# Optimization experiments

Hardware: AMD Instinct MI355X
Metric: run time of the kernel (lower is better)

The kernel has to match this reference:

```python
import jax, jax.numpy as jnp
import numpy as np

EPS = 1e-7  # K.epsilon()

def setup_inputs() -> dict:
    key = jax.random.key(0)
    k1, k2, k3 = jax.random.split(key, 3)
    B, T, D = 32, 2048, 512
    x = jax.random.normal(k1, (B, T, D), dtype=jnp.float32)
    W = jax.random.normal(k2, (D, D), dtype=jnp.float32) * (1.0 / np.sqrt(D))
    b = jnp.zeros((D,), dtype=jnp.float32)
    u = jax.random.normal(k3, (D,), dtype=jnp.float32) * (1.0 / np.sqrt(D))
    return {"x": x, "W": W, "b": b, "u": u}

def reference(x, W, b, u):
    # uit = tanh(x @ W + b)  -> [B, T, D]
    uit = jnp.tanh(jnp.einsum('btd,de->bte', x, W) + b)
    # scores: sum over feature dim of uit * u -> [B, T]
    ait = jnp.einsum('btd,d->bt', uit, u)
    # exp + normalize over T (no mask); matches original exp/sum form
    a = jnp.exp(ait)
    a = a / (jnp.sum(a, axis=1, keepdims=True) + EPS)
    # weighted sum pooling over T -> [B, D]
    return jnp.einsum('btd,bt->bd', x, a)
```

## Files before the change

### kernel.cpp

```cpp
#include <hip/hip_runtime.h>
#include <math.h>

#define D_DIM 512

typedef short short8v __attribute__((ext_vector_type(8)));
typedef unsigned short ushort8v __attribute__((ext_vector_type(8)));
typedef float f32x16 __attribute__((ext_vector_type(16)));

__device__ inline unsigned short f2bf(float f) {
    union { float f; unsigned int u; } a; a.f = f;
    unsigned int u = a.u;
    unsigned int r = (u + 0x7fffu + ((u >> 16) & 1u)) >> 16;
    return (unsigned short)r;
}

__device__ inline float fast_tanh(float y) {
    float e2 = __expf(2.f * y);
    return 1.f - __fdividef(2.f, e2 + 1.f);
}

#define ASYNC_CP16(gp, lp) \
    __builtin_amdgcn_global_load_lds( \
        (const __attribute__((address_space(1))) void*)(gp), \
        (__attribute__((address_space(3))) void*)(lp), 16, 0, 0)

__global__ __launch_bounds__(256) void wt_kernel(const float* __restrict__ W,
                                                 unsigned short* __restrict__ Wb2) {
    __shared__ __align__(16) unsigned short lbuf[16384];
    const int s = blockIdx.x;
    const int tid = threadIdx.x;
    #pragma unroll
    for (int i = 0; i < 16; ++i) {
        int flat = tid + i * 256;
        int kr = flat >> 7;
        int e4 = (flat & 127) * 4;
        float4 v = *(const float4*)(W + (size_t)(s * 32 + kr) * D_DIM + e4);
        int ks = kr >> 4, half = (kr >> 3) & 1, j = kr & 7;
        float vv[4] = {v.x, v.y, v.z, v.w};
        #pragma unroll
        for (int q = 0; q < 4; ++q) {
            int e = e4 + q, nt = e >> 5, nl = e & 31;
            lbuf[(((nt * 2 + ks) * 2 + half) * 32 + nl) * 8 + j] = f2bf(vv[q]);
        }
    }
    __syncthreads();
    #pragma unroll
    for (int i = 0; i < 8; ++i) {
        int c = tid + i * 256;
        *(ushort8v*)(Wb2 + (size_t)s * 16384 + c * 8) = *(const ushort8v*)&lbuf[c * 8];
    }
}

constexpr int XLDE = 40;

__global__ __launch_bounds__(256, 2) void gemm_ait_mfma(
    const float* __restrict__ x, const unsigned short* __restrict__ Wb2,
    const float* __restrict__ bias, const float* __restrict__ u,
    float* __restrict__ ait)
{
    __shared__ __align__(16) unsigned short wsh[2][16384];
    __shared__ __align__(16) unsigned short xs[2][64 * XLDE];
    __shared__ float rowpart[4][64];

    const int tid  = threadIdx.x;
    const int wave = tid >> 6;
    const int lane = tid & 63;
    const int half = lane >> 5;
    const int nl   = lane & 31;
    const int m0   = blockIdx.x * 64;

    f32x16 acc[2][4];
    #pragma unroll
    for (int mi = 0; mi < 2; ++mi)
        #pragma unroll
        for (int ni = 0; ni < 4; ++ni)
            #pragma unroll
            for (int r = 0; r < 16; ++r) acc[mi][ni][r] = 0.f;

    const int xr = tid >> 2;
    const int xc = tid & 3;
    const float* xbase = x + (size_t)(m0 + xr) * D_DIM + xc * 8;

    #pragma unroll
    for (int i = 0; i < 8; ++i)
        ASYNC_CP16(Wb2 + tid * 8 + i * 2048, &wsh[0][tid * 8 + i * 2048]);
    float4 px0 = *(const float4*)(xbase);
    float4 px1 = *(const float4*)(xbase + 4);

    for (int s = 0; s < 16; ++s) {
        const int pb = s & 1;
        {
            ushort8v pk;
            pk[0] = f2bf(px0.x); pk[1] = f2bf(px0.y); pk[2] = f2bf(px0.z); pk[3] = f2bf(px0.w);
            pk[4] = f2bf(px1.x); pk[5] = f2bf(px1.y); pk[6] = f2bf(px1.z); pk[7] = f2bf(px1.w);
            *(ushort8v*)&xs[pb][xr * XLDE + xc * 8] = pk;
        }
        __syncthreads();

        if (s + 1 < 16) {
            const unsigned short* wsrc = Wb2 + (size_t)(s + 1) * 16384;
            #pragma unroll
            for (int i = 0; i < 8; ++i)
                ASYNC_CP16(wsrc + tid * 8 + i * 2048, &wsh[1 - pb][tid * 8 + i * 2048]);
            px0 = *(const float4*)(xbase + (s + 1) * 32);
            px1 = *(const float4*)(xbase + (s + 1) * 32 + 4);
        }

        #pragma unroll
        for (int ks = 0; ks < 2; ++ks) {
            short8v af[2], bfr[4];
            #pragma unroll
            for (int mi = 0; mi < 2; ++mi)
                af[mi] = *(const short8v*)&xs[pb][(mi * 32 + nl) * XLDE + ks * 16 + half * 8];
            #pragma unroll
            for (int ni = 0; ni < 4; ++ni)
                bfr[ni] = *(const short8v*)&wsh[pb][(((wave * 4 + ni) * 2 + ks) * 2 + half) * 256 + nl * 8];
            #pragma unroll
            for (int mi = 0; mi < 2; ++mi)
                #pragma unroll
                for (int ni = 0; ni < 4; ++ni)
                    acc[mi][ni] = __builtin_amdgcn_mfma_f32_32x32x16_bf16(
                        af[mi], bfr[ni], acc[mi][ni], 0, 0, 0);
        }
    }

    float rowsum[2][16];
    #pragma unroll
    for (int mi = 0; mi < 2; ++mi)
        #pragma unroll
        for (int r = 0; r < 16; ++r) rowsum[mi][r] = 0.f;

    #pragma unroll
    for (int mi = 0; mi < 2; ++mi) {
        #pragma unroll
        for (int ni = 0; ni < 4; ++ni) {
            int col = wave * 128 + ni * 32 + nl;
            float be = bias[col], ue = u[col];
            #pragma unroll
            for (int r = 0; r < 16; ++r)
                rowsum[mi][r] += fast_tanh(acc[mi][ni][r] + be) * ue;
        }
    }
    #pragma unroll
    for (int mi = 0; mi < 2; ++mi)
        #pragma unroll
        for (int r = 0; r < 16; ++r) {
            float v = rowsum[mi][r];
            v += __shfl_xor(v, 1, 64);
            v += __shfl_xor(v, 2, 64);
            v += __shfl_xor(v, 4, 64);
            v += __shfl_xor(v, 8, 64);
            v += __shfl_xor(v, 16, 64);
            rowsum[mi][r] = v;
        }
    if (nl == 0) {
        #pragma unroll
        for (int mi = 0; mi < 2; ++mi)
            #pragma unroll
            for (int r = 0; r < 16; ++r) {
                int row = mi * 32 + (r & 3) + 8 * (r >> 2) + 4 * half;
                rowpart[wave][row] = rowsum[mi][r];
            }
    }
    __syncthreads();
    if (tid < 64)
        ait[m0 + tid] = rowpart[0][tid] + rowpart[1][tid] + rowpart[2][tid] + rowpart[3][tid];
}

__global__ __launch_bounds__(256) void gemm_ait_f32(
    const float* __restrict__ x, const float* __restrict__ W,
    const float* __restrict__ bias, const float* __restrict__ u,
    float* __restrict__ ait)
{
    __shared__ float xsf[64][68];
    __shared__ float wshf[64][132];
    const int tid = threadIdx.x;
    const int tx = tid & 15, ty = tid >> 4;
    const int m0 = blockIdx.x * 64;
    float rowsum[4] = {0.f, 0.f, 0.f, 0.f};
    for (int e0 = 0; e0 < D_DIM; e0 += 128) {
        float acc[4][8];
        #pragma unroll
        for (int i = 0; i < 4; ++i)
            #pragma unroll
            for (int j = 0; j < 8; ++j) acc[i][j] = 0.f;
        for (int kc = 0; kc < D_DIM; kc += 64) {
            #pragma unroll
            for (int i = 0; i < 4; ++i) {
                int idx = tid + i * 256;
                int r = idx >> 4, c = (idx & 15) * 4;
                *(float4*)&xsf[r][c] = *(const float4*)(x + (size_t)(m0 + r) * D_DIM + kc + c);
            }
            #pragma unroll
            for (int i = 0; i < 8; ++i) {
                int idx = tid + i * 256;
                int r = idx >> 5, c = (idx & 31) * 4;
                *(float4*)&wshf[r][c] = *(const float4*)(W + (size_t)(kc + r) * D_DIM + e0 + c);
            }
            __syncthreads();
            #pragma unroll 4
            for (int k = 0; k < 64; ++k) {
                float xv[4];
                #pragma unroll
                for (int i = 0; i < 4; ++i) xv[i] = xsf[ty * 4 + i][k];
                float4 w0 = *(const float4*)&wshf[k][tx * 8];
                float4 w1 = *(const float4*)&wshf[k][tx * 8 + 4];
                #pragma unroll
                for (int i = 0; i < 4; ++i) {
                    acc[i][0] += xv[i] * w0.x; acc[i][1] += xv[i] * w0.y;
                    acc[i][2] += xv[i] * w0.z; acc[i][3] += xv[i] * w0.w;
                    acc[i][4] += xv[i] * w1.x; acc[i][5] += xv[i] * w1.y;
                    acc[i][6] += xv[i] * w1.z; acc[i][7] += xv[i] * w1.w;
                }
            }
            __syncthreads();
        }
        #pragma unroll
        for (int j = 0; j < 8; ++j) {
            int e = e0 + tx * 8 + j;
            float be = bias[e], ue = u[e];
            #pragma unroll
            for (int i = 0; i < 4; ++i) rowsum[i] += tanhf(acc[i][j] + be) * ue;
        }
    }
    float* red = &xsf[0][0];
    #pragma unroll
    for (int i = 0; i < 4; ++i) red[(ty * 4 + i) * 16 + tx] = rowsum[i];
    __syncthreads();
    if (tid < 64) {
        float s = 0.f;
        #pragma unroll
        for (int j = 0; j < 16; ++j) s += red[tid * 16 + j];
        ait[m0 + tid] = s;
    }
}

__global__ __launch_bounds__(256) void softmax_kernel(float* __restrict__ ait, int T)
{
    const int b = blockIdx.x;
    float* p = ait + (size_t)b * T;
    const int tid = threadIdx.x;
    float ev[8];
    float local = 0.f;
    #pragma unroll
    for (int i = 0; i < 8; ++i) {
        ev[i] = expf(p[tid + i * 256]);
        local += ev[i];
    }
    #pragma unroll
    for (int off = 32; off > 0; off >>= 1)
        local += __shfl_down(local, off, 64);
    __shared__ float wsum[4];
    const int wv = tid >> 6, lane = tid & 63;
    if (lane == 0) wsum[wv] = local;
    __syncthreads();
    float total = wsum[0] + wsum[1] + wsum[2] + wsum[3];
    float inv = 1.0f / (total + 1e-7f);
    #pragma unroll
    for (int i = 0; i < 8; ++i) p[tid + i * 256] = ev[i] * inv;
}

__device__ inline float4 pool_accum(const float* __restrict__ x,
                                    const float* __restrict__ a,
                                    int b, int c, int tid, int T) {
    const int th = tid >> 7;
    const int d = (tid & 127) * 4;
    const float* xp = x + ((size_t)b * T + c * 64) * D_DIM + d;
    const float* ap = a + (size_t)b * T + c * 64;
    float4 acc = {0.f, 0.f, 0.f, 0.f};
    #pragma unroll 8
    for (int t = th; t < 64; t += 2) {
        float s = ap[t];
        float4 xv = *(const float4*)(xp + (size_t)t * D_DIM);
        acc.x += xv.x * s; acc.y += xv.y * s;
        acc.z += xv.z * s; acc.w += xv.w * s;
    }
    return acc;
}

__global__ __launch_bounds__(256) void pool_partial_kernel(
    const float* __restrict__ x, const float* __restrict__ a,
    float* __restrict__ partial, int T)
{
    const int chunks = T >> 6;
    const int b = blockIdx.x / chunks;
    const int c = blockIdx.x % chunks;
    const int tid = threadIdx.x;
    float4 acc = pool_accum(x, a, b, c, tid, T);
    __shared__ float4 tmp[128];
    if ((tid >> 7) == 1) tmp[tid & 127] = acc;
    __syncthreads();
    if ((tid >> 7) == 0) {
        float4 o = tmp[tid];
        acc.x += o.x; acc.y += o.y; acc.z += o.z; acc.w += o.w;
        *(float4*)(partial + (size_t)blockIdx.x * D_DIM + tid * 4) = acc;
    }
}

__global__ __launch_bounds__(256) void pool_reduce_kernel(
    const float* __restrict__ partial, float* __restrict__ out, int chunks)
{
    const int b = blockIdx.x;
    const int tid = threadIdx.x;
    const int d = tid * 2;
    float2 acc = {0.f, 0.f};
    for (int c = 0; c < chunks; ++c) {
        float2 v = *(const float2*)(partial + ((size_t)b * chunks + c) * D_DIM + d);
        acc.x += v.x; acc.y += v.y;
    }
    *(float2*)(out + (size_t)b * D_DIM + d) = acc;
}

__global__ __launch_bounds__(256) void pool_atomic_kernel(
    const float* __restrict__ x, const float* __restrict__ a,
    float* __restrict__ out, int T)
{
    const int chunks = T >> 6;
    const int b = blockIdx.x / chunks;
    const int c = blockIdx.x % chunks;
    const int tid = threadIdx.x;
    float4 acc = pool_accum(x, a, b, c, tid, T);
    __shared__ float4 tmp[128];
    if ((tid >> 7) == 1) tmp[tid & 127] = acc;
    __syncthreads();
    if ((tid >> 7) == 0) {
        float4 o = tmp[tid];
        float* op = out + (size_t)b * D_DIM + tid * 4;
        atomicAdd(op + 0, acc.x + o.x);
        atomicAdd(op + 1, acc.y + o.y);
        atomicAdd(op + 2, acc.z + o.z);
        atomicAdd(op + 3, acc.w + o.w);
    }
}

extern "C" void kernel_launch(void* const* d_in, const int* in_sizes, int n_in,
                              void* d_out, int out_size, void* d_ws, size_t ws_size,
                              hipStream_t stream)
{
    const float* x    = (const float*)d_in[0];
    const float* W    = (const float*)d_in[1];
    const float* bias = (const float*)d_in[2];
    const float* u    = (const float*)d_in[3];
    float* out = (float*)d_out;

    const int Dd = in_sizes[2];
    const int M  = in_sizes[0] / Dd;
    const int B  = out_size / Dd;
    const int T  = M / B;
    const int chunks = T >> 6;

    const size_t wb_bytes   = (size_t)Dd * Dd * sizeof(unsigned short);
    const size_t ait_bytes  = (size_t)M * sizeof(float);
    const size_t part_bytes = (size_t)B * chunks * Dd * sizeof(float);

    if (ws_size >= wb_bytes + ait_bytes) {
        unsigned short* Wb2 = (unsigned short*)d_ws;
        float* ait = (float*)((char*)d_ws + wb_bytes);
        wt_kernel<<<dim3(16), dim3(256), 0, stream>>>(W, Wb2);
        gemm_ait_mfma<<<dim3(M / 64), dim3(256), 0, stream>>>(x, Wb2, bias, u, ait);
        softmax_kernel<<<dim3(B), dim3(256), 0, stream>>>(ait, T);
        if (ws_size >= wb_bytes + ait_bytes + part_bytes) {
            float* partial = (float*)((char*)d_ws + wb_bytes + ait_bytes);
            pool_partial_kernel<<<dim3(B * chunks), dim3(256), 0, stream>>>(x, ait, partial, T);
            pool_reduce_kernel<<<dim3(B), dim3(256), 0, stream>>>(partial, out, chunks);
        } else {
            hipMemsetAsync(d_out, 0, (size_t)out_size * sizeof(float), stream);
            pool_atomic_kernel<<<dim3(B * chunks), dim3(256), 0, stream>>>(x, ait, out, T);
        }
    } else {
        float* ait = (float*)d_ws;
        gemm_ait_f32<<<dim3(M / 64), dim3(256), 0, stream>>>(x, W, bias, u, ait);
        softmax_kernel<<<dim3(B), dim3(256), 0, stream>>>(ait, T);
        hipMemsetAsync(d_out, 0, (size_t)out_size * sizeof(float), stream);
        pool_atomic_kernel<<<dim3(B * chunks), dim3(256), 0, stream>>>(x, ait, out, T);
    }
}
```

Before: 274.4 us.

## Double GEMM row tile with 2x4 wave grid and coarsen pooling chunks

The attention-score GEMM now processes 128 rows per block with 512 threads arranged as a 2x4 wave grid. Each bf16 W tile loaded into LDS is therefore shared by twice as many rows, halving redundant W traffic from L2. Pooling chunks grow from 64 to 256 timesteps, giving fewer partial sums and a cheaper reduce, and the partial buffer reuses the packed-W workspace region. The retained launch bound of 2 blocks at 512 threads may cap registers near the size of the 128-float accumulator set, which risks spills.

```diff
diff --git a/kernel.cpp b/kernel.cpp
--- a/kernel.cpp
+++ b/kernel.cpp
@@ -24,14 +24,14 @@
         (const __attribute__((address_space(1))) void*)(gp), \
         (__attribute__((address_space(3))) void*)(lp), 16, 0, 0)
 
-__global__ __launch_bounds__(256) void wt_kernel(const float* __restrict__ W,
-                                                 unsigned short* __restrict__ Wb2) {
+__global__ __launch_bounds__(1024) void wt_kernel(const float* __restrict__ W,
+                                                  unsigned short* __restrict__ Wb2) {
     __shared__ __align__(16) unsigned short lbuf[16384];
     const int s = blockIdx.x;
     const int tid = threadIdx.x;
     #pragma unroll
-    for (int i = 0; i < 16; ++i) {
-        int flat = tid + i * 256;
+    for (int i = 0; i < 4; ++i) {
+        int flat = tid + i * 1024;
         int kr = flat >> 7;
         int e4 = (flat & 127) * 4;
         float4 v = *(const float4*)(W + (size_t)(s * 32 + kr) * D_DIM + e4);
@@ -45,29 +45,31 @@
     }
     __syncthreads();
     #pragma unroll
-    for (int i = 0; i < 8; ++i) {
-        int c = tid + i * 256;
+    for (int i = 0; i < 2; ++i) {
+        int c = tid + i * 1024;
         *(ushort8v*)(Wb2 + (size_t)s * 16384 + c * 8) = *(const ushort8v*)&lbuf[c * 8];
     }
 }
 
 constexpr int XLDE = 40;
 
-__global__ __launch_bounds__(256, 2) void gemm_ait_mfma(
+__global__ __launch_bounds__(512, 2) void gemm_ait_mfma(
     const float* __restrict__ x, const unsigned short* __restrict__ Wb2,
     const float* __restrict__ bias, const float* __restrict__ u,
     float* __restrict__ ait)
 {
     __shared__ __align__(16) unsigned short wsh[2][16384];
-    __shared__ __align__(16) unsigned short xs[2][64 * XLDE];
-    __shared__ float rowpart[4][64];
+    __shared__ __align__(16) unsigned short xs[2][128 * XLDE];
+    __shared__ float rowpart[4][128];
 
     const int tid  = threadIdx.x;
     const int wave = tid >> 6;
     const int lane = tid & 63;
     const int half = lane >> 5;
     const int nl   = lane & 31;
-    const int m0   = blockIdx.x * 64;
+    const int wr   = wave >> 2;
+    const int wc   = wave & 3;
+    const int m0   = blockIdx.x * 128;
 
     f32x16 acc[2][4];
     #pragma unroll
@@ -82,8 +84,8 @@
     const float* xbase = x + (size_t)(m0 + xr) * D_DIM + xc * 8;
 
     #pragma unroll
-    for (int i = 0; i < 8; ++i)
-        ASYNC_CP16(Wb2 + tid * 8 + i * 2048, &wsh[0][tid * 8 + i * 2048]);
+    for (int i = 0; i < 4; ++i)
+        ASYNC_CP16(Wb2 + tid * 8 + i * 4096, &wsh[0][tid * 8 + i * 4096]);
     float4 px0 = *(const float4*)(xbase);
     float4 px1 = *(const float4*)(xbase + 4);
 
@@ -100,8 +102,8 @@
         if (s + 1 < 16) {
             const unsigned short* wsrc = Wb2 + (size_t)(s + 1) * 16384;
             #pragma unroll
-            for (int i = 0; i < 8; ++i)
-                ASYNC_CP16(wsrc + tid * 8 + i * 2048, &wsh[1 - pb][tid * 8 + i * 2048]);
+            for (int i = 0; i < 4; ++i)
+                ASYNC_CP16(wsrc + tid * 8 + i * 4096, &wsh[1 - pb][tid * 8 + i * 4096]);
             px0 = *(const float4*)(xbase + (s + 1) * 32);
             px1 = *(const float4*)(xbase + (s + 1) * 32 + 4);
         }
@@ -111,10 +113,10 @@
             short8v af[2], bfr[4];
             #pragma unroll
             for (int mi = 0; mi < 2; ++mi)
-                af[mi] = *(const short8v*)&xs[pb][(mi * 32 + nl) * XLDE + ks * 16 + half * 8];
+                af[mi] = *(const short8v*)&xs[pb][(wr * 64 + mi * 32 + nl) * XLDE + ks * 16 + half * 8];
             #pragma unroll
             for (int ni = 0; ni < 4; ++ni)
-                bfr[ni] = *(const short8v*)&wsh[pb][(((wave * 4 + ni) * 2 + ks) * 2 + half) * 256 + nl * 8];
+                bfr[ni] = *(const short8v*)&wsh[pb][(((wc * 4 + ni) * 2 + ks) * 2 + half) * 256 + nl * 8];
             #pragma unroll
             for (int mi = 0; mi < 2; ++mi)
                 #pragma unroll
@@ -134,7 +136,7 @@
     for (int mi = 0; mi < 2; ++mi) {
         #pragma unroll
         for (int ni = 0; ni < 4; ++ni) {
-            int col = wave * 128 + ni * 32 + nl;
+            int col = wc * 128 + ni * 32 + nl;
             float be = bias[col], ue = u[col];
             #pragma unroll
             for (int r = 0; r < 16; ++r)
@@ -158,12 +160,12 @@
         for (int mi = 0; mi < 2; ++mi)
             #pragma unroll
             for (int r = 0; r < 16; ++r) {
-                int row = mi * 32 + (r & 3) + 8 * (r >> 2) + 4 * half;
-                rowpart[wave][row] = rowsum[mi][r];
+                int row = wr * 64 + mi * 32 + (r & 3) + 8 * (r >> 2) + 4 * half;
+                rowpart[wc][row] = rowsum[mi][r];
             }
     }
     __syncthreads();
-    if (tid < 64)
+    if (tid < 128)
         ait[m0 + tid] = rowpart[0][tid] + rowpart[1][tid] + rowpart[2][tid] + rowpart[3][tid];
 }
 
@@ -260,37 +262,32 @@
     for (int i = 0; i < 8; ++i) p[tid + i * 256] = ev[i] * inv;
 }
 
-__device__ inline float4 pool_accum(const float* __restrict__ x,
-                                    const float* __restrict__ a,
-                                    int b, int c, int tid, int T) {
+__global__ __launch_bounds__(256) void pool_partial_kernel(
+    const float* __restrict__ x, const float* __restrict__ a,
+    float* __restrict__ partial, int T)
+{
+    const int chunks = T >> 8;
+    const int b = blockIdx.x / chunks;
+    const int c = blockIdx.x % chunks;
+    const int tid = threadIdx.x;
     const int th = tid >> 7;
     const int d = (tid & 127) * 4;
-    const float* xp = x + ((size_t)b * T + c * 64) * D_DIM + d;
-    const float* ap = a + (size_t)b * T + c * 64;
+
+    const float* xp = x + ((size_t)b * T + c * 256) * D_DIM + d;
+    const float* ap = a + (size_t)b * T + c * 256;
+
     float4 acc = {0.f, 0.f, 0.f, 0.f};
     #pragma unroll 8
-    for (int t = th; t < 64; t += 2) {
+    for (int t = th; t < 256; t += 2) {
         float s = ap[t];
         float4 xv = *(const float4*)(xp + (size_t)t * D_DIM);
         acc.x += xv.x * s; acc.y += xv.y * s;
         acc.z += xv.z * s; acc.w += xv.w * s;
     }
-    return acc;
-}
-
-__global__ __launch_bounds__(256) void pool_partial_kernel(
-    const float* __restrict__ x, const float* __restrict__ a,
-    float* __restrict__ partial, int T)
-{
-    const int chunks = T >> 6;
-    const int b = blockIdx.x / chunks;
-    const int c = blockIdx.x % chunks;
-    const int tid = threadIdx.x;
-    float4 acc = pool_accum(x, a, b, c, tid, T);
     __shared__ float4 tmp[128];
-    if ((tid >> 7) == 1) tmp[tid & 127] = acc;
-    __syncthreads();
-    if ((tid >> 7) == 0) {
+    if (th == 1) tmp[tid & 127] = acc;
+    __syncthreads();
+    if (th == 0) {
         float4 o = tmp[tid];
         acc.x += o.x; acc.y += o.y; acc.z += o.z; acc.w += o.w;
         *(float4*)(partial + (size_t)blockIdx.x * D_DIM + tid * 4) = acc;
@@ -315,15 +312,26 @@
     const float* __restrict__ x, const float* __restrict__ a,
     float* __restrict__ out, int T)
 {
-    const int chunks = T >> 6;
+    const int chunks = T >> 8;
     const int b = blockIdx.x / chunks;
     const int c = blockIdx.x % chunks;
     const int tid = threadIdx.x;
-    float4 acc = pool_accum(x, a, b, c, tid, T);
+    const int th = tid >> 7;
+    const int d = (tid & 127) * 4;
+    const float* xp = x + ((size_t)b * T + c * 256) * D_DIM + d;
+    const float* ap = a + (size_t)b * T + c * 256;
+    float4 acc = {0.f, 0.f, 0.f, 0.f};
+    #pragma unroll 8
+    for (int t = th; t < 256; t += 2) {
+        float s = ap[t];
+        float4 xv = *(const float4*)(xp + (size_t)t * D_DIM);
+        acc.x += xv.x * s; acc.y += xv.y * s;
+        acc.z += xv.z * s; acc.w += xv.w * s;
+    }
     __shared__ float4 tmp[128];
-    if ((tid >> 7) == 1) tmp[tid & 127] = acc;
-    __syncthreads();
-    if ((tid >> 7) == 0) {
+    if (th == 1) tmp[tid & 127] = acc;
+    __syncthreads();
+    if (th == 0) {
         float4 o = tmp[tid];
         float* op = out + (size_t)b * D_DIM + tid * 4;
         atomicAdd(op + 0, acc.x + o.x);
@@ -347,26 +355,21 @@
     const int M  = in_sizes[0] / Dd;
     const int B  = out_size / Dd;
     const int T  = M / B;
-    const int chunks = T >> 6;
-
-    const size_t wb_bytes   = (size_t)Dd * Dd * sizeof(unsigned short);
-    const size_t ait_bytes  = (size_t)M * sizeof(float);
-    const size_t part_bytes = (size_t)B * chunks * Dd * sizeof(float);
+    const int chunks = T >> 8;
+
+    const size_t wb_bytes  = (size_t)Dd * Dd * sizeof(unsigned short);
+    const size_t ait_bytes = (size_t)M * sizeof(float);
 
     if (ws_size >= wb_bytes + ait_bytes) {
         unsigned short* Wb2 = (unsigned short*)d_ws;
-        float* ait = (float*)((char*)d_ws + wb_bytes);
-        wt_kernel<<<dim3(16), dim3(256), 0, stream>>>(W, Wb2);
-        gemm_ait_mfma<<<dim3(M / 64), dim3(256), 0, stream>>>(x, Wb2, bias, u, ait);
+        float* ait     = (float*)((char*)d_ws + wb_bytes);
+        float* partial = (float*)d_ws;
+
+        wt_kernel<<<dim3(16), dim3(1024), 0, stream>>>(W, Wb2);
+        gemm_ait_mfma<<<dim3(M / 128), dim3(512), 0, stream>>>(x, Wb2, bias, u, ait);
         softmax_kernel<<<dim3(B), dim3(256), 0, stream>>>(ait, T);
-        if (ws_size >= wb_bytes + ait_bytes + part_bytes) {
-            float* partial = (float*)((char*)d_ws + wb_bytes + ait_bytes);
-            pool_partial_kernel<<<dim3(B * chunks), dim3(256), 0, stream>>>(x, ait, partial, T);
-            pool_reduce_kernel<<<dim3(B), dim3(256), 0, stream>>>(partial, out, chunks);
-        } else {
-            hipMemsetAsync(d_out, 0, (size_t)out_size * sizeof(float), stream);
-            pool_atomic_kernel<<<dim3(B * chunks), dim3(256), 0, stream>>>(x, ait, out, T);
-        }
+        pool_partial_kernel<<<dim3(B * chunks), dim3(256), 0, stream>>>(x, ait, partial, T);
+        pool_reduce_kernel<<<dim3(B), dim3(256), 0, stream>>>(partial, out, chunks);
     } else {
         float* ait = (float*)d_ws;
         gemm_ait_f32<<<dim3(M / 64), dim3(256), 0, stream>>>(x, W, bias, u, ait);
```

Result: faster. 260.1 us (-5.2%).
